# Kernel optimization log

Measured on AMD Instinct MI355X. Metric: run time of the kernel, lower is better.

Reference implementation:

```python
import jax, jax.numpy as jnp
import numpy as np
from jax import lax

B, L, D_MODEL = 2, 1024, 1024
EXPAND, D_STATE, D_CONV = 2, 16, 4
D_INNER = EXPAND * D_MODEL
DT_RANK = D_MODEL // 16  # ceil(1024/16) = 64
D_FF = 4 * D_MODEL


def setup_inputs() -> dict:
    key = jax.random.key(0)
    ks = jax.random.split(key, 20)
    s = lambda *sh: 1.0 / np.sqrt(sh[-1])
    inp = {
        "x": jax.random.normal(ks[0], (B, L, D_MODEL), jnp.float32),
        "ln1_w": jnp.ones((D_MODEL,), jnp.float32),
        "ln1_b": jnp.zeros((D_MODEL,), jnp.float32),
        "W_in": jax.random.normal(ks[1], (2 * D_INNER, D_MODEL), jnp.float32) * s(D_MODEL),
        "conv_w": jax.random.normal(ks[2], (D_INNER, D_CONV), jnp.float32) * s(D_CONV),
        "conv_b": jnp.zeros((D_INNER,), jnp.float32),
        "W_xproj": jax.random.normal(ks[3], (DT_RANK + 2 * D_STATE, D_INNER), jnp.float32) * s(D_INNER),
        "W_dt": jax.random.normal(ks[4], (D_INNER, DT_RANK), jnp.float32) * s(DT_RANK),
        "b_dt": jax.random.uniform(ks[5], (D_INNER,), jnp.float32, -4.0, -2.0),  # dt bias ~ small softplus
        "A_log": jnp.log(jnp.broadcast_to(jnp.arange(1, D_STATE + 1, dtype=jnp.float32), (D_INNER, D_STATE))),
        "D": jnp.ones((D_INNER,), jnp.float32),
        "W_out": jax.random.normal(ks[6], (D_MODEL, D_INNER), jnp.float32) * s(D_INNER),
        "ln2_w": jnp.ones((D_MODEL,), jnp.float32),
        "ln2_b": jnp.zeros((D_MODEL,), jnp.float32),
        "W1": jax.random.normal(ks[7], (D_FF, D_MODEL), jnp.float32) * s(D_MODEL),
        "b1": jnp.zeros((D_FF,), jnp.float32),
        "W2": jax.random.normal(ks[8], (D_MODEL, D_FF), jnp.float32) * s(D_FF),
        "b2": jnp.zeros((D_MODEL,), jnp.float32),
    }
    return inp


def _layernorm(x, w, b, eps=1e-5):
    mu = jnp.mean(x, axis=-1, keepdims=True)
    var = jnp.var(x, axis=-1, keepdims=True)
    return (x - mu) * lax.rsqrt(var + eps) * w + b


def _mamba(h, W_in, conv_w, conv_b, W_xproj, W_dt, b_dt, A_log, D, W_out):
    # in_proj -> [B, L, 2*d_inner]
    xz = jnp.einsum("bld,ed->ble", h, W_in)
    u, z = xz[..., :D_INNER], xz[..., D_INNER:]
    # causal depthwise conv over time
    uc = jnp.transpose(u, (0, 2, 1))  # [B, d_inner, L]
    uc = lax.conv_general_dilated(
        uc, conv_w[:, None, :], window_strides=(1,), padding=[(D_CONV - 1, 0)],
        dimension_numbers=("NCH", "OIH", "NCH"), feature_group_count=D_INNER)
    uc = jax.nn.silu(uc + conv_b[None, :, None])
    u = jnp.transpose(uc, (0, 2, 1))  # [B, L, d_inner]
    # input-dependent dt, B, C
    x_db = jnp.einsum("bld,ed->ble", u, W_xproj)
    dt = jax.nn.softplus(jnp.einsum("blr,dr->bld", x_db[..., :DT_RANK], W_dt) + b_dt)
    Bm = x_db[..., DT_RANK:DT_RANK + D_STATE]  # [B, L, d_state]
    Cm = x_db[..., DT_RANK + D_STATE:]         # [B, L, d_state]
    A = -jnp.exp(A_log)                        # [d_inner, d_state]

    def step(hst, t):
        dt_t, B_t, C_t, u_t = t  # [B,d_inner], [B,ds], [B,ds], [B,d_inner]
        dA = jnp.exp(dt_t[:, :, None] * A)                       # [B,d_inner,d_state]
        hst = dA * hst + dt_t[:, :, None] * B_t[:, None, :] * u_t[:, :, None]
        y_t = jnp.einsum("bds,bs->bd", hst, C_t)
        return hst, y_t

    h0 = jnp.zeros((u.shape[0], D_INNER, D_STATE), u.dtype)
    xs = (jnp.swapaxes(dt, 0, 1), jnp.swapaxes(Bm, 0, 1), jnp.swapaxes(Cm, 0, 1), jnp.swapaxes(u, 0, 1))
    _, ys = lax.scan(step, h0, xs)
    y = jnp.swapaxes(ys, 0, 1) + u * D  # skip term D*u
    y = y * jax.nn.silu(z)
    return jnp.einsum("ble,de->bld", y, W_out)


def reference(x, ln1_w, ln1_b, W_in, conv_w, conv_b, W_xproj, W_dt, b_dt, A_log, D,
              W_out, ln2_w, ln2_b, W1, b1, W2, b2):
    x = x + _mamba(_layernorm(x, ln1_w, ln1_b), W_in, conv_w, conv_b, W_xproj, W_dt, b_dt, A_log, D, W_out)
    h = _layernorm(x, ln2_w, ln2_b)
    ffn = jnp.einsum("blf,df->bld", jax.nn.relu(jnp.einsum("bld,fd->blf", h, W1) + b1), W2) + b2
    return x + ffn
```

## Files before the change

### kernel.cpp

```cpp
#include <hip/hip_runtime.h>

typedef unsigned short u16;
typedef unsigned int   u32;
typedef short   bf16x8 __attribute__((ext_vector_type(8)));
typedef float   f32x4  __attribute__((ext_vector_type(4)));
typedef u16     u16x4  __attribute__((ext_vector_type(4)));

__device__ __forceinline__ u16 f2b(float f) {
    u32 u = __builtin_bit_cast(u32, f);
    u32 r = u + 0x7FFFu + ((u >> 16) & 1u);
    return (u16)(r >> 16);
}
__device__ __forceinline__ float b2f(u16 h) {
    u32 u = ((u32)h) << 16;
    return __builtin_bit_cast(float, u);
}
__device__ __forceinline__ u16x4 f4_to_b4(float4 v) {
    u16x4 o; o.x = f2b(v.x); o.y = f2b(v.y); o.z = f2b(v.z); o.w = f2b(v.w);
    return o;
}

__device__ __forceinline__ float fexp2(float x) {
    float r;
    asm("v_exp_f32 %0, %1" : "=v"(r) : "v"(x));
    return r;
}

template <int CTRL>
__device__ __forceinline__ float dpp_add(float p) {
    int pi = __builtin_bit_cast(int, p);
    int q  = __builtin_amdgcn_update_dpp(pi, pi, CTRL, 0xF, 0xF, false);
    return p + __builtin_bit_cast(float, q);
}
#define DPP_XOR1 0xB1
#define DPP_XOR2 0x4E
#define DPP_HMIR 0x141
#define DPP_MIR  0x140

#define MROWS   2048
#define NSEG    16
#define SEGT    64
#define L2E     1.44269504088896340736f

#define GLDS(g, l) __builtin_amdgcn_global_load_lds(                      \
    (const __attribute__((address_space(1))) void*)(g),                   \
    (__attribute__((address_space(3))) void*)(l), 16, 0, 0)

__global__ __launch_bounds__(256) void cvt_kernel(const float* __restrict__ in,
                                                  u16* __restrict__ out, int n4) {
    int i = blockIdx.x * 256 + threadIdx.x;
    if (i < n4) {
        float4 v = ((const float4*)in)[i];
        ((u16x4*)out)[i] = f4_to_b4(v);
    }
}

__global__ __launch_bounds__(256) void pad_xproj_kernel(const float* __restrict__ in,
                                                        u16* __restrict__ out) {
    int i = blockIdx.x * 256 + threadIdx.x;
    int r = i >> 9, c4 = i & 511;
    float4 v = make_float4(0.f, 0.f, 0.f, 0.f);
    if (r < 96) v = ((const float4*)(in + (size_t)r * 2048))[c4];
    ((u16x4*)(out + (size_t)r * 2048))[c4] = f4_to_b4(v);
}

__global__ __launch_bounds__(256) void ln_kernel(const float* __restrict__ x,
                                                 const float* __restrict__ w,
                                                 const float* __restrict__ b,
                                                 u16* __restrict__ out) {
    const int row = blockIdx.x;
    const int tid = threadIdx.x;
    const float4 v = ((const float4*)(x + (size_t)row * 1024))[tid];
    float s = v.x + v.y + v.z + v.w;
    float q = v.x * v.x + v.y * v.y + v.z * v.z + v.w * v.w;
#pragma unroll
    for (int off = 1; off < 64; off <<= 1) {
        s += __shfl_xor(s, off, 64);
        q += __shfl_xor(q, off, 64);
    }
    __shared__ float ss[4], qq[4];
    const int wave = tid >> 6;
    if ((tid & 63) == 0) { ss[wave] = s; qq[wave] = q; }
    __syncthreads();
    s = ss[0] + ss[1] + ss[2] + ss[3];
    q = qq[0] + qq[1] + qq[2] + qq[3];
    const float mean = s * (1.f / 1024.f);
    const float var  = q * (1.f / 1024.f) - mean * mean;
    const float rstd = rsqrtf(var + 1e-5f);
    const float4 wv = ((const float4*)w)[tid];
    const float4 bv = ((const float4*)b)[tid];
    float4 o;
    o.x = (v.x - mean) * rstd * wv.x + bv.x;
    o.y = (v.y - mean) * rstd * wv.y + bv.y;
    o.z = (v.z - mean) * rstd * wv.z + bv.z;
    o.w = (v.w - mean) * rstd * wv.w + bv.w;
    ((u16x4*)(out + (size_t)row * 1024))[tid] = f4_to_b4(o);
}

__global__ __launch_bounds__(256) void conv_kernel(const float* __restrict__ xzu,
                                                   const float* __restrict__ cw,
                                                   const float* __restrict__ cb,
                                                   u16* __restrict__ up) {
    const int idx = blockIdx.x * 256 + threadIdx.x;
    const int row = idx >> 9;
    const int d4  = idx & 511;
    const int d   = d4 * 4;
    const int bb  = row >> 10;
    const int t   = row & 1023;
    float w0[4], w1[4], w2[4], w3[4];
    *(float4*)w0 = ((const float4*)cw)[d + 0];
    *(float4*)w1 = ((const float4*)cw)[d + 1];
    *(float4*)w2 = ((const float4*)cw)[d + 2];
    *(float4*)w3 = ((const float4*)cw)[d + 3];
    float4 a = ((const float4*)cb)[d4];
#pragma unroll
    for (int j = 0; j < 4; ++j) {
        const int tt = t - 3 + j;
        if (tt >= 0) {
            const float4 uv = *(const float4*)(xzu + ((size_t)(bb * 1024 + tt)) * 2048 + d);
            a.x += uv.x * w0[j];
            a.y += uv.y * w1[j];
            a.z += uv.z * w2[j];
            a.w += uv.w * w3[j];
        }
    }
    float4 o;
    o.x = a.x / (1.f + __expf(-a.x));
    o.y = a.y / (1.f + __expf(-a.y));
    o.z = a.z / (1.f + __expf(-a.z));
    o.w = a.w / (1.f + __expf(-a.w));
    ((u16x4*)up)[idx] = f4_to_b4(o);
}

template <int EPI>
__global__ __launch_bounds__(256) void gemm_tb(const u16* __restrict__ A,
                                               const u16* __restrict__ Bw,
                                               void* __restrict__ Cptr,
                                               void* __restrict__ Cptr2,
                                               const float* __restrict__ bias,
                                               int M, int N, int K, int KS) {
    __shared__ u16 Asm[3][128 * 32];
    __shared__ u16 Bsm[3][128 * 32];
    const int tid  = threadIdx.x;
    const int bm   = blockIdx.x, bn = blockIdx.y, kz = blockIdx.z;
    const int lane = tid & 63;
    const int wave = tid >> 6;
    const int wm   = wave >> 1, wn = wave & 1;
    const u16* Ag = A  + (size_t)bm * 128 * K;
    const u16* Bg = Bw + (size_t)bn * 128 * K;
    const int r0 = tid >> 2;
    const int r1 = r0 + 64;
    const int sg = (tid & 3) * 8;
    const int k0 = kz * KS;
    const int nk = KS >> 5;
    const int fr = lane & 15, fk = (lane >> 4) * 8;

#define STG(bf, kk)                                                            \
    {                                                                          \
        const int kof = k0 + (kk) * 32;                                        \
        GLDS(Ag + (size_t)r0 * K + kof + sg, &Asm[bf][tid * 8]);               \
        GLDS(Ag + (size_t)r1 * K + kof + sg, &Asm[bf][(tid + 256) * 8]);       \
        GLDS(Bg + (size_t)r0 * K + kof + sg, &Bsm[bf][tid * 8]);               \
        GLDS(Bg + (size_t)r1 * K + kof + sg, &Bsm[bf][(tid + 256) * 8]);       \
    }

    f32x4 acc[4][4] = {};
    STG(0, 0); STG(1, 1); STG(2, 2);
    int buf = 0;
    for (int k = 0; k < nk; ++k) {
        if (k < nk - 2)       asm volatile("s_waitcnt vmcnt(8)" ::: "memory");
        else if (k == nk - 2) asm volatile("s_waitcnt vmcnt(4)" ::: "memory");
        else                  asm volatile("s_waitcnt vmcnt(0)" ::: "memory");
        __builtin_amdgcn_s_barrier();
        bf16x8 a[4], b[4];
#pragma unroll
        for (int m = 0; m < 4; ++m)
            a[m] = *(const bf16x8*)&Asm[buf][(wm * 64 + m * 16 + fr) * 32 + fk];
#pragma unroll
        for (int n = 0; n < 4; ++n)
            b[n] = *(const bf16x8*)&Bsm[buf][(wn * 64 + n * 16 + fr) * 32 + fk];
        asm volatile("s_waitcnt lgkmcnt(0)" ::: "memory");
        __builtin_amdgcn_s_barrier();
        if (k + 3 < nk) STG(buf, k + 3);
#pragma unroll
        for (int m = 0; m < 4; ++m)
#pragma unroll
            for (int n = 0; n < 4; ++n)
                acc[m][n] = __builtin_amdgcn_mfma_f32_16x16x32_bf16(a[m], b[n], acc[m][n], 0, 0, 0);
        buf = (buf == 2) ? 0 : buf + 1;
    }
#undef STG

    const int fq = lane >> 4;
#pragma unroll
    for (int m = 0; m < 4; ++m) {
#pragma unroll
        for (int n = 0; n < 4; ++n) {
            const int row0 = bm * 128 + wm * 64 + m * 16 + fq * 4;
            const int col  = bn * 128 + wn * 64 + n * 16 + fr;
#pragma unroll
            for (int j = 0; j < 4; ++j) {
                float v = acc[m][n][j];
                if constexpr (EPI == 3) {
                    v += bias[col];
                    ((u16*)Cptr)[(size_t)(row0 + j) * N + col] = f2b(fmaxf(v, 0.f));
                } else if constexpr (EPI == 5) {
                    if (col < 2048) {
                        ((float*)Cptr)[(size_t)(row0 + j) * 2048 + col] = v;
                    } else {
                        const float sv = v / (1.f + __expf(-v));
                        ((u16*)Cptr2)[(size_t)(row0 + j) * 2048 + col - 2048] = f2b(sv);
                    }
                } else {
                    ((float*)Cptr)[(size_t)kz * M * N + (size_t)(row0 + j) * N + col] = v;
                }
            }
        }
    }
}

__global__ __launch_bounds__(256) void xproj_combine(const float* __restrict__ part,
                                                     u16* __restrict__ xdbr,
                                                     float* __restrict__ bcp) {
    int i = blockIdx.x * 256 + threadIdx.x;
    int row = i >> 5, c4 = i & 31;
    if (c4 >= 24) return;
    float4 s = make_float4(0.f, 0.f, 0.f, 0.f);
#pragma unroll
    for (int p = 0; p < 8; ++p) {
        float4 v = ((const float4*)(part + (size_t)p * MROWS * 128 + (size_t)row * 128))[c4];
        s.x += v.x; s.y += v.y; s.z += v.z; s.w += v.w;
    }
    if (c4 < 16) {
        ((u16x4*)(xdbr + (size_t)row * 64))[c4] = f4_to_b4(s);
    } else {
        const int e0 = (c4 - 16) * 4;
        float sv[4] = {s.x, s.y, s.z, s.w};
#pragma unroll
        for (int j = 0; j < 4; ++j) {
            const int e = e0 + j;
            const int st  = (e < 16) ? e : (e - 16);
            const int isc = (e < 16) ? 0 : 1;
            bcp[(size_t)(row >> 1) * 64 + st * 4 + (row & 1) * 2 + isc] = sv[j];
        }
    }
}

__device__ __forceinline__ void compute_dtu_tile(const u16* __restrict__ xdbr,
                                                 const u16* __restrict__ Wdtb,
                                                 const float* __restrict__ b_dt,
                                                 const u16* __restrict__ u,
                                                 float* __restrict__ du_s,
                                                 size_t t0, int d0, int w, int l) {
    const int fr = l & 15, fk = (l >> 4) * 8;
    const bf16x8 a0 = *(const bf16x8*)(xdbr + (t0 + w * 16 + fr) * 64 + fk);
    const bf16x8 a1 = *(const bf16x8*)(xdbr + (t0 + w * 16 + fr) * 64 + 32 + fk);
    const bf16x8 b0 = *(const bf16x8*)(Wdtb + (size_t)(d0 + fr) * 64 + fk);
    const bf16x8 b1 = *(const bf16x8*)(Wdtb + (size_t)(d0 + fr) * 64 + 32 + fk);
    const float bdt = b_dt[d0 + fr];
    f32x4 acc = {};
    acc = __builtin_amdgcn_mfma_f32_16x16x32_bf16(a0, b0, acc, 0, 0, 0);
    acc = __builtin_amdgcn_mfma_f32_16x16x32_bf16(a1, b1, acc, 0, 0, 0);
#pragma unroll
    for (int j = 0; j < 4; ++j) {
        const int row = w * 16 + (l >> 4) * 4 + j;
        float v = acc[j] + bdt;
        v = (v > 20.f) ? v : log1pf(__expf(v));
        const float uval = b2f(u[(t0 + row) * 2048 + d0 + fr]);
        float2 dv; dv.x = v; dv.y = v * uval;
        *(float2*)&du_s[(row >> 1) * 66 + fr * 4 + (row & 1) * 2] = dv;
    }
}

__device__ __forceinline__ void stage_bc(const float* __restrict__ bcp,
                                         float* __restrict__ bc_s,
                                         size_t p0, int w, int l) {
    const int pr = (w << 3) + (l >> 4);
    const int pc = (l & 15) << 2;
    GLDS(bcp + (p0 + pr) * 64 + pc,     &bc_s[(w << 9)]);
    GLDS(bcp + (p0 + pr + 4) * 64 + pc, &bc_s[(w << 9) + 256]);
}

__global__ __launch_bounds__(256) void scan_pass1(const u16* __restrict__ xdbr,
                                                  const u16* __restrict__ Wdtb,
                                                  const float* __restrict__ b_dt,
                                                  const u16* __restrict__ u,
                                                  const float* __restrict__ bcp,
                                                  const float* __restrict__ A_log,
                                                  float* __restrict__ Qarr,
                                                  float* __restrict__ Sarr) {
    __shared__ __align__(16) float du_s[32 * 66];
    __shared__ __align__(16) float bc_s[32 * 64];

    const int tid = threadIdx.x;
    const int l   = tid & 63;
    const int w   = tid >> 6;
    const int s   = l & 15;
    const int g   = (w << 2) | (l >> 4);
    const int d0  = blockIdx.x << 4;
    const int b   = blockIdx.y;
    const int seg = blockIdx.z;
    const int d   = d0 + g;
    const size_t t0 = (size_t)b * 1024 + (size_t)seg * SEGT;

    stage_bc(bcp, bc_s, t0 >> 1, w, l);
    compute_dtu_tile(xdbr, Wdtb, b_dt, u, du_s, t0, d0, w, l);

    const float As2 = -__expf(A_log[d * 16 + s]) * L2E;
    asm volatile("s_waitcnt vmcnt(0) lgkmcnt(0)" ::: "memory");
    __builtin_amdgcn_s_barrier();

    float Q = 0.f, S = 0.f;
#pragma unroll 8
    for (int t2 = 0; t2 < 32; ++t2) {
        const float4 du4 = *(const float4*)&du_s[t2 * 66 + g * 4];
        const float4 BC2 = *(const float4*)&bc_s[t2 * 64 + s * 4];
        S += du4.x;
        Q = fexp2(du4.x * As2) * Q + du4.y * BC2.x;
        S += du4.z;
        Q = fexp2(du4.z * As2) * Q + du4.w * BC2.z;
    }
    Qarr[(((size_t)seg * 2 + b) * 2048 + d) * 16 + s] = Q;
    if (s == 0) Sarr[((size_t)seg * 2 + b) * 2048 + d] = S;
}

__global__ __launch_bounds__(256) void scan_prefix(const float* __restrict__ Qarr,
                                                   const float* __restrict__ Sarr,
                                                   const float* __restrict__ A_log,
                                                   float* __restrict__ H0) {
    const int tid = threadIdx.x;
    const int d   = (blockIdx.x << 4) + (tid >> 4);
    const int s   = tid & 15;
    const int b   = blockIdx.y;
    const float As2 = -__expf(A_log[d * 16 + s]) * L2E;
    float h = 0.f;
#pragma unroll
    for (int i = 0; i < NSEG; ++i) {
        const size_t base = ((size_t)i * 2 + b) * 2048 + d;
        H0[base * 16 + s] = h;
        h = fexp2(As2 * Sarr[base]) * h + Qarr[base * 16 + s];
    }
}

__global__ __launch_bounds__(256) void scan_pass2(const u16* __restrict__ xdbr,
                                                  const u16* __restrict__ Wdtb,
                                                  const float* __restrict__ b_dt,
                                                  const u16* __restrict__ u,
                                                  const float* __restrict__ bcp,
                                                  const u16* __restrict__ zsil,
                                                  const float* __restrict__ A_log,
                                                  const float* __restrict__ Dp,
                                                  const float* __restrict__ H0,
                                                  u16* __restrict__ ymul) {
    __shared__ __align__(16) float du_s[32 * 66];
    __shared__ __align__(16) float bc_s[32 * 64];
    __shared__ __align__(16) float p_s[1024];

    const int tid = threadIdx.x;
    const int l   = tid & 63;
    const int w   = tid >> 6;
    const int s   = l & 15;
    const int g   = (w << 2) | (l >> 4);
    const int d0  = blockIdx.x << 4;
    const int b   = blockIdx.y;
    const int seg = blockIdx.z;
    const int d   = d0 + g;
    const size_t t0 = (size_t)b * 1024 + (size_t)seg * SEGT;

    stage_bc(bcp, bc_s, t0 >> 1, w, l);
    compute_dtu_tile(xdbr, Wdtb, b_dt, u, du_s, t0, d0, w, l);

    const float As2 = -__expf(A_log[d * 16 + s]) * L2E;
    float h = H0[(((size_t)seg * 2 + b) * 2048 + d) * 16 + s];

    asm volatile("s_waitcnt vmcnt(0) lgkmcnt(0)" ::: "memory");
    __builtin_amdgcn_s_barrier();

    float pk[4];
#pragma unroll
    for (int c = 0; c < 4; ++c) {
        pk[c] = 0.f;
#pragma unroll
        for (int q = 0; q < 8; ++q) {
            const int t2 = c * 8 + q;
            const float4 du4 = *(const float4*)&du_s[t2 * 66 + g * 4];
            const float4 BC2 = *(const float4*)&bc_s[t2 * 64 + s * 4];
            h = fexp2(du4.x * As2) * h + du4.y * BC2.x;
            float p = h * BC2.y;
            p = dpp_add<DPP_XOR1>(p);
            p = dpp_add<DPP_XOR2>(p);
            p = dpp_add<DPP_HMIR>(p);
            p = dpp_add<DPP_MIR>(p);
            {
                const unsigned long long km = 0x0001000100010001ULL << (2 * q);
                asm("v_cndmask_b32 %0, %0, %1, %2" : "+v"(pk[c]) : "v"(p), "s"(km));
            }
            h = fexp2(du4.z * As2) * h + du4.w * BC2.z;
            p = h * BC2.w;
            p = dpp_add<DPP_XOR1>(p);
            p = dpp_add<DPP_XOR2>(p);
            p = dpp_add<DPP_HMIR>(p);
            p = dpp_add<DPP_MIR>(p);
            {
                const unsigned long long km = 0x0001000100010001ULL << (2 * q + 1);
                asm("v_cndmask_b32 %0, %0, %1, %2" : "+v"(pk[c]) : "v"(p), "s"(km));
            }
        }
    }
#pragma unroll
    for (int c = 0; c < 4; ++c) {
        const int row = c * 16 + s;
        p_s[row * 16 + (g ^ (row & 12))] = pk[c];
    }

    asm volatile("s_waitcnt lgkmcnt(0)" ::: "memory");
    __builtin_amdgcn_s_barrier();

    {
        const int tt = tid >> 2, cc = (tid & 3) << 2;
        const float4 pv = *(const float4*)&p_s[tt * 16 + (cc ^ (tt & 12))];
        const u16x4  uv = *(const u16x4*)(u + (t0 + tt) * 2048 + d0 + cc);
        const u16x4  zs = *(const u16x4*)(zsil + (t0 + tt) * 2048 + d0 + cc);
        const float4 Dv = *(const float4*)(Dp + d0 + cc);
        float4 o;
        o.x = (pv.x + b2f(uv.x) * Dv.x) * b2f(zs.x);
        o.y = (pv.y + b2f(uv.y) * Dv.y) * b2f(zs.y);
        o.z = (pv.z + b2f(uv.z) * Dv.z) * b2f(zs.z);
        o.w = (pv.w + b2f(uv.w) * Dv.w) * b2f(zs.w);
        *(u16x4*)(ymul + (t0 + tt) * 2048 + d0 + cc) = f4_to_b4(o);
    }
}

__global__ __launch_bounds__(256) void ffn2_combine(const float* __restrict__ part,
                                                    const float* __restrict__ x2,
                                                    const float* __restrict__ b2,
                                                    float* __restrict__ out) {
    int i = blockIdx.x * 256 + threadIdx.x;
    float4 s = ((const float4*)x2)[i];
    float4 bv = ((const float4*)b2)[i & 255];
    s.x += bv.x; s.y += bv.y; s.z += bv.z; s.w += bv.w;
#pragma unroll
    for (int p = 0; p < 4; ++p) {
        float4 v = ((const float4*)(part + (size_t)p * MROWS * 1024))[i];
        s.x += v.x; s.y += v.y; s.z += v.z; s.w += v.w;
    }
    ((float4*)out)[i] = s;
}

__global__ __launch_bounds__(256) void outproj_combine_ln2(const float* __restrict__ x,
                                                           const float* __restrict__ part,
                                                           const float* __restrict__ w,
                                                           const float* __restrict__ b,
                                                           float* __restrict__ x2,
                                                           u16* __restrict__ h2) {
    const int row = blockIdx.x;
    const int tid = threadIdx.x;
    float4 v = ((const float4*)(x + (size_t)row * 1024))[tid];
    float4 p0 = ((const float4*)(part + (size_t)row * 1024))[tid];
    float4 p1 = ((const float4*)(part + (size_t)MROWS * 1024 + (size_t)row * 1024))[tid];
    v.x += p0.x + p1.x; v.y += p0.y + p1.y; v.z += p0.z + p1.z; v.w += p0.w + p1.w;
    ((float4*)(x2 + (size_t)row * 1024))[tid] = v;
    float s = v.x + v.y + v.z + v.w;
    float q = v.x * v.x + v.y * v.y + v.z * v.z + v.w * v.w;
#pragma unroll
    for (int off = 1; off < 64; off <<= 1) {
        s += __shfl_xor(s, off, 64);
        q += __shfl_xor(q, off, 64);
    }
    __shared__ float ss[4], qq[4];
    const int wave = tid >> 6;
    if ((tid & 63) == 0) { ss[wave] = s; qq[wave] = q; }
    __syncthreads();
    s = ss[0] + ss[1] + ss[2] + ss[3];
    q = qq[0] + qq[1] + qq[2] + qq[3];
    const float mean = s * (1.f / 1024.f);
    const float var  = q * (1.f / 1024.f) - mean * mean;
    const float rstd = rsqrtf(var + 1e-5f);
    const float4 wv = ((const float4*)w)[tid];
    const float4 bv = ((const float4*)b)[tid];
    float4 o;
    o.x = (v.x - mean) * rstd * wv.x + bv.x;
    o.y = (v.y - mean) * rstd * wv.y + bv.y;
    o.z = (v.z - mean) * rstd * wv.z + bv.z;
    o.w = (v.w - mean) * rstd * wv.w + bv.w;
    ((u16x4*)(h2 + (size_t)row * 1024))[tid] = f4_to_b4(o);
}

extern "C" void kernel_launch(void* const* d_in, const int* in_sizes, int n_in,
                              void* d_out, int out_size, void* d_ws, size_t ws_size,
                              hipStream_t stream) {
    const float* x      = (const float*)d_in[0];
    const float* ln1_w  = (const float*)d_in[1];
    const float* ln1_b  = (const float*)d_in[2];
    const float* W_in   = (const float*)d_in[3];
    const float* conv_w = (const float*)d_in[4];
    const float* conv_b = (const float*)d_in[5];
    const float* W_xproj= (const float*)d_in[6];
    const float* W_dt   = (const float*)d_in[7];
    const float* b_dt   = (const float*)d_in[8];
    const float* A_log  = (const float*)d_in[9];
    const float* Dvec   = (const float*)d_in[10];
    const float* W_out  = (const float*)d_in[11];
    const float* ln2_w  = (const float*)d_in[12];
    const float* ln2_b  = (const float*)d_in[13];
    const float* W1     = (const float*)d_in[14];
    const float* b1     = (const float*)d_in[15];
    const float* W2     = (const float*)d_in[16];
    const float* b2     = (const float*)d_in[17];
    float* out = (float*)d_out;
    char*  ws  = (char*)d_ws;
    const size_t MB = 1024ull * 1024ull;

    u16*   h1b   = (u16*)(ws + 0);
    float* xzu   = (float*)(ws + 4 * MB);
    u16*   zsil  = (u16*)(ws + 20 * MB);
    u16*   upb   = (u16*)(ws + 28 * MB);
    float* parts = (float*)(ws + 36 * MB);
    float* bcp   = (float*)(ws + 44 * MB);
    u16*   xdbr  = (u16*)(ws + 44 * MB + 256 * 1024);
    u16*   Wdtb  = (u16*)(ws + 44 * MB + 512 * 1024);
    u16*   ymul  = (u16*)(ws + 45 * MB);
    float* Qarr  = (float*)(ws + 53 * MB);
    float* Sarr  = (float*)(ws + 57 * MB);
    float* H0    = (float*)(ws + 58 * MB);
    float* x2    = (float*)(ws + 62 * MB);
    u16*   Winb  = (u16*)(ws + 70 * MB);
    u16*   Woutb = (u16*)(ws + 78 * MB);
    u16*   W1b   = (u16*)(ws + 82 * MB);
    u16*   W2b   = (u16*)(ws + 90 * MB);
    u16*   Wxpb  = (u16*)(ws + 98 * MB);
    u16*   h2b   = h1b;
    float* opart = (float*)(ws + 4 * MB);
    u16*   f1    = (u16*)(ws + 4 * MB);
    float* fpart = (float*)(ws + 20 * MB);

    cvt_kernel<<<4096, 256, 0, stream>>>(W_in,  Winb,  4096 * 1024 / 4);
    cvt_kernel<<<2048, 256, 0, stream>>>(W_out, Woutb, 1024 * 2048 / 4);
    cvt_kernel<<<4096, 256, 0, stream>>>(W1,    W1b,   4096 * 1024 / 4);
    cvt_kernel<<<4096, 256, 0, stream>>>(W2,    W2b,   1024 * 4096 / 4);
    cvt_kernel<<<128,  256, 0, stream>>>(W_dt,  Wdtb,  2048 * 64 / 4);
    pad_xproj_kernel<<<256, 256, 0, stream>>>(W_xproj, Wxpb);

    ln_kernel<<<2048, 256, 0, stream>>>(x, ln1_w, ln1_b, h1b);
    gemm_tb<5><<<dim3(16, 32, 1), 256, 0, stream>>>(h1b, Winb, xzu, zsil, nullptr,
                                                    MROWS, 4096, 1024, 1024);
    conv_kernel<<<4096, 256, 0, stream>>>(xzu, conv_w, conv_b, upb);
    gemm_tb<10><<<dim3(16, 1, 8), 256, 0, stream>>>(upb, Wxpb, parts, nullptr, nullptr,
                                                    MROWS, 128, 2048, 256);
    xproj_combine<<<256, 256, 0, stream>>>(parts, xdbr, bcp);
    scan_pass1<<<dim3(128, 2, NSEG), 256, 0, stream>>>(xdbr, Wdtb, b_dt, upb, bcp, A_log,
                                                       Qarr, Sarr);
    scan_prefix<<<dim3(128, 2), 256, 0, stream>>>(Qarr, Sarr, A_log, H0);
    scan_pass2<<<dim3(128, 2, NSEG), 256, 0, stream>>>(xdbr, Wdtb, b_dt, upb, bcp, zsil,
                                                       A_log, Dvec, H0, ymul);
    gemm_tb<10><<<dim3(16, 8, 2), 256, 0, stream>>>(ymul, Woutb, opart, nullptr, nullptr,
                                                    MROWS, 1024, 2048, 1024);
    outproj_combine_ln2<<<2048, 256, 0, stream>>>(x, opart, ln2_w, ln2_b, x2, h2b);
    gemm_tb<3><<<dim3(16, 32, 1), 256, 0, stream>>>(h2b, W1b, f1, nullptr, b1,
                                                    MROWS, 4096, 1024, 1024);
    gemm_tb<10><<<dim3(16, 8, 4), 256, 0, stream>>>(f1, W2b, fpart, nullptr, nullptr,
                                                    MROWS, 1024, 4096, 1024);
    ffn2_combine<<<2048, 256, 0, stream>>>(fpart, x2, b2, out);
}
```

Baseline: 250.4 us.

## Tile u and silu(z) by 16-channel groups, swizzle GEMM blocks, fast softplus

```diff
diff --git a/kernel.cpp b/kernel.cpp
--- a/kernel.cpp
+++ b/kernel.cpp
@@ -25,6 +25,11 @@
     asm("v_exp_f32 %0, %1" : "=v"(r) : "v"(x));
     return r;
 }
+__device__ __forceinline__ float flog2(float x) {
+    float r;
+    asm("v_log_f32 %0, %1" : "=v"(r) : "v"(x));
+    return r;
+}
 
 template <int CTRL>
 __device__ __forceinline__ float dpp_add(float p) {
@@ -41,6 +46,7 @@
 #define NSEG    16
 #define SEGT    64
 #define L2E     1.44269504088896340736f
+#define LN2     0.69314718055994530942f
 
 #define GLDS(g, l) __builtin_amdgcn_global_load_lds(                      \
     (const __attribute__((address_space(1))) void*)(g),                   \
@@ -100,7 +106,8 @@
 __global__ __launch_bounds__(256) void conv_kernel(const float* __restrict__ xzu,
                                                    const float* __restrict__ cw,
                                                    const float* __restrict__ cb,
-                                                   u16* __restrict__ up) {
+                                                   u16* __restrict__ up,
+                                                   u16* __restrict__ utl) {
     const int idx = blockIdx.x * 256 + threadIdx.x;
     const int row = idx >> 9;
     const int d4  = idx & 511;
@@ -129,7 +136,9 @@
     o.y = a.y / (1.f + __expf(-a.y));
     o.z = a.z / (1.f + __expf(-a.z));
     o.w = a.w / (1.f + __expf(-a.w));
-    ((u16x4*)up)[idx] = f4_to_b4(o);
+    const u16x4 pk = f4_to_b4(o);
+    ((u16x4*)up)[idx] = pk;
+    *(u16x4*)(utl + (((size_t)(d >> 4)) * 2048 + row) * 16 + (d & 15)) = pk;
 }
 
 template <int EPI>
@@ -139,10 +148,16 @@
                                                void* __restrict__ Cptr2,
                                                const float* __restrict__ bias,
                                                int M, int N, int K, int KS) {
+    const int nbm = gridDim.x, nbn = gridDim.y;
+    const int nwg = nbm * nbn;
+    const int id  = blockIdx.x + nbm * blockIdx.y;
+    const int sw  = (id & 7) * (nwg >> 3) + (id >> 3);
+    const int bm  = sw % nbm, bn = sw / nbm;
+
     __shared__ u16 Asm[3][128 * 32];
     __shared__ u16 Bsm[3][128 * 32];
     const int tid  = threadIdx.x;
-    const int bm   = blockIdx.x, bn = blockIdx.y, kz = blockIdx.z;
+    const int kz   = blockIdx.z;
     const int lane = tid & 63;
     const int wave = tid >> 6;
     const int wm   = wave >> 1, wn = wave & 1;
@@ -209,7 +224,9 @@
                         ((float*)Cptr)[(size_t)(row0 + j) * 2048 + col] = v;
                     } else {
                         const float sv = v / (1.f + __expf(-v));
-                        ((u16*)Cptr2)[(size_t)(row0 + j) * 2048 + col - 2048] = f2b(sv);
+                        const int zc = col - 2048;
+                        ((u16*)Cptr2)[(((size_t)(zc >> 4)) * 2048 + row0 + j) * 16 + (zc & 15)]
+                            = f2b(sv);
                     }
                 } else {
                     ((float*)Cptr)[(size_t)kz * M * N + (size_t)(row0 + j) * N + col] = v;
@@ -249,7 +266,7 @@
 __device__ __forceinline__ void compute_dtu_tile(const u16* __restrict__ xdbr,
                                                  const u16* __restrict__ Wdtb,
                                                  const float* __restrict__ b_dt,
-                                                 const u16* __restrict__ u,
+                                                 const u16* __restrict__ utile,
                                                  float* __restrict__ du_s,
                                                  size_t t0, int d0, int w, int l) {
     const int fr = l & 15, fk = (l >> 4) * 8;
@@ -265,8 +282,9 @@
     for (int j = 0; j < 4; ++j) {
         const int row = w * 16 + (l >> 4) * 4 + j;
         float v = acc[j] + bdt;
-        v = (v > 20.f) ? v : log1pf(__expf(v));
-        const float uval = b2f(u[(t0 + row) * 2048 + d0 + fr]);
+        const float sp = flog2(1.f + fexp2(v * L2E)) * LN2;
+        v = (v > 20.f) ? v : sp;
+        const float uval = b2f(utile[(t0 + row) * 16 + fr]);
         float2 dv; dv.x = v; dv.y = v * uval;
         *(float2*)&du_s[(row >> 1) * 66 + fr * 4 + (row & 1) * 2] = dv;
     }
@@ -284,7 +302,7 @@
 __global__ __launch_bounds__(256) void scan_pass1(const u16* __restrict__ xdbr,
                                                   const u16* __restrict__ Wdtb,
                                                   const float* __restrict__ b_dt,
-                                                  const u16* __restrict__ u,
+                                                  const u16* __restrict__ utl,
                                                   const float* __restrict__ bcp,
                                                   const float* __restrict__ A_log,
                                                   float* __restrict__ Qarr,
@@ -302,9 +320,10 @@
     const int seg = blockIdx.z;
     const int d   = d0 + g;
     const size_t t0 = (size_t)b * 1024 + (size_t)seg * SEGT;
+    const u16* utile = utl + (size_t)(d0 >> 4) * 2048 * 16;
 
     stage_bc(bcp, bc_s, t0 >> 1, w, l);
-    compute_dtu_tile(xdbr, Wdtb, b_dt, u, du_s, t0, d0, w, l);
+    compute_dtu_tile(xdbr, Wdtb, b_dt, utile, du_s, t0, d0, w, l);
 
     const float As2 = -__expf(A_log[d * 16 + s]) * L2E;
     asm volatile("s_waitcnt vmcnt(0) lgkmcnt(0)" ::: "memory");
@@ -345,16 +364,17 @@
 __global__ __launch_bounds__(256) void scan_pass2(const u16* __restrict__ xdbr,
                                                   const u16* __restrict__ Wdtb,
                                                   const float* __restrict__ b_dt,
-                                                  const u16* __restrict__ u,
+                                                  const u16* __restrict__ utl,
                                                   const float* __restrict__ bcp,
-                                                  const u16* __restrict__ zsil,
+                                                  const u16* __restrict__ zst,
                                                   const float* __restrict__ A_log,
                                                   const float* __restrict__ Dp,
                                                   const float* __restrict__ H0,
                                                   u16* __restrict__ ymul) {
     __shared__ __align__(16) float du_s[32 * 66];
     __shared__ __align__(16) float bc_s[32 * 64];
-    __shared__ __align__(16) float p_s[1024];
+    __shared__ __align__(16) u16   u_s[1024];
+    __shared__ __align__(16) u16   z_s[1024];
 
     const int tid = threadIdx.x;
     const int l   = tid & 63;
@@ -366,9 +386,16 @@
     const int seg = blockIdx.z;
     const int d   = d0 + g;
     const size_t t0 = (size_t)b * 1024 + (size_t)seg * SEGT;
+    const u16* utile = utl + (size_t)(d0 >> 4) * 2048 * 16;
+    const u16* ztile = zst + (size_t)(d0 >> 4) * 2048 * 16;
 
     stage_bc(bcp, bc_s, t0 >> 1, w, l);
-    compute_dtu_tile(xdbr, Wdtb, b_dt, u, du_s, t0, d0, w, l);
+    if (w < 2)
+        GLDS(utile + t0 * 16 + ((w & 1) * 64 + l) * 8, &u_s[(w & 1) << 9]);
+    else
+        GLDS(ztile + t0 * 16 + ((w & 1) * 64 + l) * 8, &z_s[(w & 1) << 9]);
+
+    compute_dtu_tile(xdbr, Wdtb, b_dt, utile, du_s, t0, d0, w, l);
 
     const float As2 = -__expf(A_log[d * 16 + s]) * L2E;
     float h = H0[(((size_t)seg * 2 + b) * 2048 + d) * 16 + s];
@@ -407,6 +434,9 @@
             }
         }
     }
+
+    __builtin_amdgcn_s_barrier();
+    float* p_s = du_s;
 #pragma unroll
     for (int c = 0; c < 4; ++c) {
         const int row = c * 16 + s;
@@ -419,8 +449,8 @@
     {
         const int tt = tid >> 2, cc = (tid & 3) << 2;
         const float4 pv = *(const float4*)&p_s[tt * 16 + (cc ^ (tt & 12))];
-        const u16x4  uv = *(const u16x4*)(u + (t0 + tt) * 2048 + d0 + cc);
-        const u16x4  zs = *(const u16x4*)(zsil + (t0 + tt) * 2048 + d0 + cc);
+        const u16x4  uv = *(const u16x4*)&u_s[tt * 16 + cc];
+        const u16x4  zs = *(const u16x4*)&z_s[tt * 16 + cc];
         const float4 Dv = *(const float4*)(Dp + d0 + cc);
         float4 o;
         o.x = (pv.x + b2f(uv.x) * Dv.x) * b2f(zs.x);
@@ -513,22 +543,23 @@
 
     u16*   h1b   = (u16*)(ws + 0);
     float* xzu   = (float*)(ws + 4 * MB);
-    u16*   zsil  = (u16*)(ws + 20 * MB);
+    u16*   zst   = (u16*)(ws + 20 * MB);
     u16*   upb   = (u16*)(ws + 28 * MB);
-    float* parts = (float*)(ws + 36 * MB);
-    float* bcp   = (float*)(ws + 44 * MB);
-    u16*   xdbr  = (u16*)(ws + 44 * MB + 256 * 1024);
-    u16*   Wdtb  = (u16*)(ws + 44 * MB + 512 * 1024);
-    u16*   ymul  = (u16*)(ws + 45 * MB);
-    float* Qarr  = (float*)(ws + 53 * MB);
-    float* Sarr  = (float*)(ws + 57 * MB);
-    float* H0    = (float*)(ws + 58 * MB);
-    float* x2    = (float*)(ws + 62 * MB);
-    u16*   Winb  = (u16*)(ws + 70 * MB);
-    u16*   Woutb = (u16*)(ws + 78 * MB);
-    u16*   W1b   = (u16*)(ws + 82 * MB);
-    u16*   W2b   = (u16*)(ws + 90 * MB);
-    u16*   Wxpb  = (u16*)(ws + 98 * MB);
+    u16*   utl   = (u16*)(ws + 36 * MB);
+    float* parts = (float*)(ws + 44 * MB);
+    float* bcp   = (float*)(ws + 52 * MB);
+    u16*   xdbr  = (u16*)(ws + 52 * MB + 256 * 1024);
+    u16*   Wdtb  = (u16*)(ws + 52 * MB + 512 * 1024);
+    u16*   ymul  = (u16*)(ws + 53 * MB);
+    float* Qarr  = (float*)(ws + 61 * MB);
+    float* Sarr  = (float*)(ws + 65 * MB);
+    float* H0    = (float*)(ws + 66 * MB);
+    float* x2    = (float*)(ws + 70 * MB);
+    u16*   Winb  = (u16*)(ws + 78 * MB);
+    u16*   Woutb = (u16*)(ws + 86 * MB);
+    u16*   W1b   = (u16*)(ws + 90 * MB);
+    u16*   W2b   = (u16*)(ws + 98 * MB);
+    u16*   Wxpb  = (u16*)(ws + 106 * MB);
     u16*   h2b   = h1b;
     float* opart = (float*)(ws + 4 * MB);
     u16*   f1    = (u16*)(ws + 4 * MB);
@@ -542,16 +573,16 @@
     pad_xproj_kernel<<<256, 256, 0, stream>>>(W_xproj, Wxpb);
 
     ln_kernel<<<2048, 256, 0, stream>>>(x, ln1_w, ln1_b, h1b);
-    gemm_tb<5><<<dim3(16, 32, 1), 256, 0, stream>>>(h1b, Winb, xzu, zsil, nullptr,
+    gemm_tb<5><<<dim3(16, 32, 1), 256, 0, stream>>>(h1b, Winb, xzu, zst, nullptr,
                                                     MROWS, 4096, 1024, 1024);
-    conv_kernel<<<4096, 256, 0, stream>>>(xzu, conv_w, conv_b, upb);
+    conv_kernel<<<4096, 256, 0, stream>>>(xzu, conv_w, conv_b, upb, utl);
     gemm_tb<10><<<dim3(16, 1, 8), 256, 0, stream>>>(upb, Wxpb, parts, nullptr, nullptr,
                                                     MROWS, 128, 2048, 256);
     xproj_combine<<<256, 256, 0, stream>>>(parts, xdbr, bcp);
-    scan_pass1<<<dim3(128, 2, NSEG), 256, 0, stream>>>(xdbr, Wdtb, b_dt, upb, bcp, A_log,
+    scan_pass1<<<dim3(128, 2, NSEG), 256, 0, stream>>>(xdbr, Wdtb, b_dt, utl, bcp, A_log,
                                                        Qarr, Sarr);
     scan_prefix<<<dim3(128, 2), 256, 0, stream>>>(Qarr, Sarr, A_log, H0);
-    scan_pass2<<<dim3(128, 2, NSEG), 256, 0, stream>>>(xdbr, Wdtb, b_dt, upb, bcp, zsil,
+    scan_pass2<<<dim3(128, 2, NSEG), 256, 0, stream>>>(xdbr, Wdtb, b_dt, utl, bcp, zst,
                                                        A_log, Dvec, H0, ymul);
     gemm_tb<10><<<dim3(16, 8, 2), 256, 0, stream>>>(ymul, Woutb, opart, nullptr, nullptr,
                                                     MROWS, 1024, 2048, 1024);
```

Result: faster. 234.7 us (-6.2%).
